# Optimization experiments

Hardware: AMD Instinct MI355X
Metric: run time of the kernel (lower is better)

The kernel has to match this reference:

```python
import jax, jax.numpy as jnp
import numpy as np

B, HIS, SIG, DIM, K = 16, 50, 512, 256, 8


def setup_inputs() -> dict:
    key = jax.random.key(0)
    ks = jax.random.split(key, 10)
    f = jax.random.normal
    return {
        "news_selection_embedding": f(ks[0], (B, HIS, SIG, DIM), jnp.float32),
        "news_embedding": f(ks[1], (B, HIS, SIG, DIM), jnp.float32),
        "user_repr": f(ks[2], (B, 1, DIM), jnp.float32),
        "news_repr": f(ks[3], (B, HIS, DIM), jnp.float32),
        "his_attn_mask": jax.random.randint(ks[4], (B, HIS, SIG), 0, 2, jnp.int32),
        "his_refined_mask": jax.random.randint(ks[5], (B, HIS, SIG), 0, 2, jnp.int32),
        "W_align": f(ks[6], (DIM, 2 * DIM), jnp.float32) * 0.05,
        "b_align": jnp.zeros((DIM,), jnp.float32),
        "sep_embedding": f(ks[7], (1, 1, 1, DIM), jnp.float32),
        "order_embedding": f(ks[8], (HIS, 1, DIM), jnp.float32),
    }


def _l2norm(x, axis):
    # F.normalize: x / clamp_min(||x||, 1e-12)
    n = jnp.linalg.norm(x, axis=axis, keepdims=True)
    return x / jnp.maximum(n, 1e-12)


def reference(news_selection_embedding, news_embedding, user_repr, news_repr,
              his_attn_mask, his_refined_mask, W_align, b_align,
              sep_embedding, order_embedding):
    Bs, H, S, D = news_embedding.shape
    # drop the leading [CLS]-style token
    sel = news_selection_embedding[:, :, 1:]          # [B,H,S-1,D]
    emb = news_embedding[:, :, 1:]                    # [B,H,S-1,D]

    # diversify: selection query from concat(user, news) through Linear(2D->D)
    nu = jnp.concatenate([jnp.broadcast_to(user_repr, news_repr.shape), news_repr], axis=-1)
    query = nu @ W_align.T + b_align                  # [B,H,D]

    # cosine similarity scores
    scores = jnp.einsum('bhsd,bhd->bhs', _l2norm(sel, -1), _l2norm(query, -1))

    # keep first k tokens always selectable; mask padded positions
    keep_k = jnp.zeros((1, S), scores.dtype).at[:, :K + 1].set(1.0)
    pad_pos = (his_refined_mask.astype(scores.dtype) + keep_k)[:, :, 1:] == 0
    scores = jnp.where(pad_pos, -jnp.inf, scores)

    score_k, kid = jax.lax.top_k(scores, K)           # [B,H,K]

    # dual gather: embeddings and attention mask
    ps_terms = jnp.take_along_axis(emb, kid[..., None], axis=2)             # [B,H,K,D]
    ps_term_mask = jnp.take_along_axis(
        his_attn_mask[:, :, 1:].astype(scores.dtype), kid, axis=-1)         # [B,H,K]

    # softmax weighting (threshold == -inf path)
    ps_terms = ps_terms * jax.nn.softmax(score_k, axis=-1)[..., None]

    # order embedding + [SEP] per article, flatten, drop trailing sep
    ps_terms = ps_terms + order_embedding             # [H,1,D] broadcast
    sep = jnp.broadcast_to(sep_embedding, (Bs, H, 1, D))
    ps_terms = jnp.concatenate([ps_terms, sep], axis=2).reshape(Bs, -1, D)[:, :-1]
    ones = jnp.ones((Bs, H, 1), ps_term_mask.dtype)
    ps_term_mask = jnp.concatenate([ps_term_mask, ones], axis=-1).reshape(Bs, -1)[:, :-1]
    return ps_terms, ps_term_mask, kid
```

## Files before the change

kernel.cpp:

```cpp
#include <hip/hip_runtime.h>
#include <math.h>

constexpr int NB  = 16;
constexpr int NH  = 50;
constexpr int NS  = 512;
constexpr int ND  = 256;
constexpr int NK  = 8;
constexpr int SM1 = NS - 1;
constexpr int ROWS = NH * (NK + 1) - 1;
constexpr int HB  = 5;
constexpr int CHUNKS = 4;
constexpr int RPC = 128;

template<int CTRL>
__device__ __forceinline__ float dpp_add(float v) {
    const int p = __builtin_amdgcn_update_dpp(0, __float_as_int(v), CTRL, 0xF, 0xF, true);
    return v + __int_as_float(p);
}

__device__ __forceinline__ float dpp_reduce16(float v) {
    v = dpp_add<0xB1>(v);
    v = dpp_add<0x4E>(v);
    v = dpp_add<0x141>(v);
    v = dpp_add<0x140>(v);
    return v;
}

__device__ __forceinline__ float4 ntload4(const float* p) {
    typedef float f4v __attribute__((ext_vector_type(4)));
    const f4v v = __builtin_nontemporal_load((const f4v*)p);
    float4 r; r.x = v.x; r.y = v.y; r.z = v.z; r.w = v.w;
    return r;
}

__global__ __launch_bounds__(256) void query_kernel(
    const float* __restrict__ user,
    const float* __restrict__ news_repr,
    const float* __restrict__ W,
    const float* __restrict__ bal,
    float* __restrict__ qn)
{
    __shared__ float us[ND];
    __shared__ float nr[HB][ND];
    __shared__ float qv_s[HB][ND];
    __shared__ float red[4];

    const int blk = blockIdx.x;
    const int b   = blk / (NH / HB);
    const int h0  = (blk % (NH / HB)) * HB;
    const int tid = threadIdx.x;
    const int ql  = tid & 15;
    const int q   = tid >> 4;

    us[tid] = user[b * ND + tid];
    #pragma unroll
    for (int i = 0; i < HB; ++i)
        nr[i][tid] = news_repr[((size_t)(b * NH + h0 + i)) * ND + tid];
    __syncthreads();

    for (int p = 0; p < 16; ++p) {
        const int d = p * 16 + q;
        const float* wrow = W + (size_t)d * (2 * ND);
        float pu = 0.f;
        float pa[HB];
        #pragma unroll
        for (int j = 0; j < HB; ++j) pa[j] = 0.f;

        #pragma unroll
        for (int i = 0; i < 4; ++i) {
            const int e = ql * 4 + 64 * i;
            const float4 wv = *(const float4*)(wrow + e);
            const float4 xv = *(const float4*)(us + e);
            pu += wv.x * xv.x + wv.y * xv.y + wv.z * xv.z + wv.w * xv.w;
        }
        #pragma unroll
        for (int i = 0; i < 4; ++i) {
            const int e = ql * 4 + 64 * i;
            const float4 wv = *(const float4*)(wrow + ND + e);
            #pragma unroll
            for (int j = 0; j < HB; ++j) {
                const float4 xv = *(const float4*)(&nr[j][e]);
                pa[j] += wv.x * xv.x + wv.y * xv.y + wv.z * xv.z + wv.w * xv.w;
            }
        }

        pu = dpp_reduce16(pu);
        #pragma unroll
        for (int j = 0; j < HB; ++j) pa[j] = dpp_reduce16(pa[j]);

        if (ql == 0) {
            const float base = bal[d] + pu;
            #pragma unroll
            for (int j = 0; j < HB; ++j) qv_s[j][d] = base + pa[j];
        }
    }
    __syncthreads();

    const int lane = tid & 63, wv_ = tid >> 6;
    for (int j = 0; j < HB; ++j) {
        const float v = qv_s[j][tid];
        float sq = v * v;
        #pragma unroll
        for (int m = 1; m < 64; m <<= 1) sq += __shfl_xor(sq, m, 64);
        if (lane == 0) red[wv_] = sq;
        __syncthreads();
        const float tot = red[0] + red[1] + red[2] + red[3];
        __syncthreads();
        qn[((size_t)(b * NH + h0 + j)) * ND + tid] = v / fmaxf(sqrtf(tot), 1e-12f);
    }
}

__global__ __launch_bounds__(256, 8) void score_kernel(
    const float* __restrict__ sel,
    const float* __restrict__ qn,
    float* __restrict__ scw)
{
    __shared__ float qs[ND];

    const int blk   = blockIdx.x;
    const int bh    = blk >> 2;
    const int chunk = blk & (CHUNKS - 1);
    const int j0    = chunk * RPC;
    const int tid   = threadIdx.x;
    const int ql    = tid & 15;
    const int q     = tid >> 4;

    qs[tid] = qn[(size_t)bh * ND + tid];
    __syncthreads();

    const float* base_bh = sel + (size_t)bh * NS * ND;

    #pragma unroll 2
    for (int it = 0; it < 8; ++it) {
        const int j = j0 + q + it * 16;
        const bool valid = (j < SM1);
        const int s = valid ? (j + 1) : SM1;
        const float* row = base_bh + (size_t)s * ND;
        float dot = 0.f, nrm = 0.f;
        #pragma unroll
        for (int i = 0; i < 4; ++i) {
            const float4 v  = ntload4(row + i * 64 + ql * 4);
            const float4 qv = *(const float4*)(qs + i * 64 + ql * 4);
            dot += v.x * qv.x + v.y * qv.y + v.z * qv.z + v.w * qv.w;
            nrm += v.x * v.x + v.y * v.y + v.z * v.z + v.w * v.w;
        }
        dot = dpp_reduce16(dot);
        nrm = dpp_reduce16(nrm);

        if (valid && ql == 0)
            scw[(size_t)bh * NS + j] = dot / fmaxf(sqrtf(nrm), 1e-12f);
    }
}

__global__ __launch_bounds__(64) void topk_out_kernel(
    const float* __restrict__ emb,
    const int*   __restrict__ attn,
    const int*   __restrict__ refined,
    const float* __restrict__ scw,
    const float* __restrict__ sep,
    const float* __restrict__ orde,
    float* __restrict__ out_terms,
    float* __restrict__ out_mask,
    float* __restrict__ out_kid)
{
    const int bh   = blockIdx.x;
    const int b    = bh / NH, h = bh % NH;
    const int lane = threadIdx.x;

    float v[8];
    {
        const float4 a = *(const float4*)(scw + (size_t)bh * NS + lane * 8);
        const float4 c = *(const float4*)(scw + (size_t)bh * NS + lane * 8 + 4);
        v[0] = a.x; v[1] = a.y; v[2] = a.z; v[3] = a.w;
        v[4] = c.x; v[5] = c.y; v[6] = c.z; v[7] = c.w;
    }
    #pragma unroll
    for (int t = 0; t < 8; ++t) {
        const int j = lane * 8 + t;
        if (j >= SM1)
            v[t] = -INFINITY;
        else if (j >= NK && refined[(size_t)bh * NS + j + 1] == 0)
            v[t] = -INFINITY;
    }

    float topv[NK];
    int   topi[NK];
    int   myi = 0;
    #pragma unroll
    for (int k = 0; k < NK; ++k) {
        float bv = -INFINITY; int bi = 0x7fffffff;
        #pragma unroll
        for (int t = 0; t < 8; ++t)
            if (v[t] > bv) { bv = v[t]; bi = lane * 8 + t; }
        #pragma unroll
        for (int m = 1; m < 64; m <<= 1) {
            const float ov = __shfl_xor(bv, m, 64);
            const int   oi = __shfl_xor(bi, m, 64);
            if (ov > bv || (ov == bv && oi < bi)) { bv = ov; bi = oi; }
        }
        topv[k] = bv; topi[k] = bi;
        if (lane == k) myi = bi;
        #pragma unroll
        for (int t = 0; t < 8; ++t)
            if (lane * 8 + t == bi) v[t] = -INFINITY;
    }

    float wk[NK], ssum = 0.f;
    #pragma unroll
    for (int k = 0; k < NK; ++k) { wk[k] = expf(topv[k] - topv[0]); ssum += wk[k]; }
    const float inv = 1.f / ssum;

    const int d4 = lane * 4;
    const float4 ord4 = *(const float4*)(orde + (size_t)h * ND + d4);
    float* obase = out_terms + ((size_t)b * ROWS + h * (NK + 1)) * ND;
    #pragma unroll
    for (int k = 0; k < NK; ++k) {
        const int s = topi[k] + 1;
        const float4 e = *(const float4*)(emb + ((size_t)bh * NS + s) * ND + d4);
        const float w = wk[k] * inv;
        float4 o;
        o.x = e.x * w + ord4.x;
        o.y = e.y * w + ord4.y;
        o.z = e.z * w + ord4.z;
        o.w = e.w * w + ord4.w;
        *(float4*)(obase + k * ND + d4) = o;
    }
    const bool has_sep = h < NH - 1;
    if (has_sep)
        *(float4*)(obase + NK * ND + d4) = *(const float4*)(sep + d4);

    if (lane < NK) {
        out_mask[(size_t)b * ROWS + h * (NK + 1) + lane] =
            (float)attn[(size_t)bh * NS + myi + 1];
        out_kid[(size_t)bh * NK + lane] = (float)myi;
    }
    if (lane == NK && has_sep)
        out_mask[(size_t)b * ROWS + h * (NK + 1) + NK] = 1.0f;
}

extern "C" void kernel_launch(void* const* d_in, const int* in_sizes, int n_in,
                              void* d_out, int out_size, void* d_ws, size_t ws_size,
                              hipStream_t stream) {
    const float* sel   = (const float*)d_in[0];
    const float* emb   = (const float*)d_in[1];
    const float* user  = (const float*)d_in[2];
    const float* nrp   = (const float*)d_in[3];
    const int*   attn  = (const int*)d_in[4];
    const int*   refin = (const int*)d_in[5];
    const float* W     = (const float*)d_in[6];
    const float* bal   = (const float*)d_in[7];
    const float* sep   = (const float*)d_in[8];
    const float* orde  = (const float*)d_in[9];

    float* qn  = (float*)d_ws;
    float* scw = qn + (size_t)NB * NH * ND;

    float* out_terms = (float*)d_out;
    float* out_mask  = out_terms + (size_t)NB * ROWS * ND;
    float* out_kid   = out_mask + (size_t)NB * ROWS;

    query_kernel<<<NB * (NH / HB), 256, 0, stream>>>(user, nrp, W, bal, qn);
    score_kernel<<<NB * NH * CHUNKS, 256, 0, stream>>>(sel, qn, scw);
    topk_out_kernel<<<NB * NH, 64, 0, stream>>>(emb, attn, refin, scw, sep, orde,
                                                out_terms, out_mask, out_kid);
}
```

Baseline: 94.21 us.

## Fuse query projection, scoring, top-k and gather into one per-head kernel

Replaces the three launches (query matvec, chunked cosine scoring, top-k/gather) with a single kernel that runs one 256-thread block per (batch, history) pair. Scores stay in shared memory instead of a workspace round-trip, and the query norm is folded into each score as one multiply. The aim is to drop the launch gaps and the intermediate global traffic. In exchange, each block now reads the whole W matrix on its own, where before one read served five heads, and the score phase runs with a quarter as many blocks, with fewer loads in flight to stream the large selection tensor.

```diff
diff --git a/kernel.cpp b/kernel.cpp
--- a/kernel.cpp
+++ b/kernel.cpp
@@ -8,9 +8,6 @@
 constexpr int NK  = 8;
 constexpr int SM1 = NS - 1;
 constexpr int ROWS = NH * (NK + 1) - 1;
-constexpr int HB  = 5;
-constexpr int CHUNKS = 4;
-constexpr int RPC = 128;
 
 template<int CTRL>
 __device__ __forceinline__ float dpp_add(float v) {
@@ -33,209 +30,167 @@
     return r;
 }
 
-__global__ __launch_bounds__(256) void query_kernel(
+__global__ __launch_bounds__(256, 8) void fused_kernel(
+    const float* __restrict__ sel,
+    const float* __restrict__ emb,
     const float* __restrict__ user,
-    const float* __restrict__ news_repr,
+    const float* __restrict__ nrp,
+    const int*   __restrict__ attn,
+    const int*   __restrict__ refined,
     const float* __restrict__ W,
     const float* __restrict__ bal,
-    float* __restrict__ qn)
-{
-    __shared__ float us[ND];
-    __shared__ float nr[HB][ND];
-    __shared__ float qv_s[HB][ND];
-    __shared__ float red[4];
-
-    const int blk = blockIdx.x;
-    const int b   = blk / (NH / HB);
-    const int h0  = (blk % (NH / HB)) * HB;
-    const int tid = threadIdx.x;
-    const int ql  = tid & 15;
-    const int q   = tid >> 4;
-
-    us[tid] = user[b * ND + tid];
-    #pragma unroll
-    for (int i = 0; i < HB; ++i)
-        nr[i][tid] = news_repr[((size_t)(b * NH + h0 + i)) * ND + tid];
-    __syncthreads();
-
-    for (int p = 0; p < 16; ++p) {
-        const int d = p * 16 + q;
-        const float* wrow = W + (size_t)d * (2 * ND);
-        float pu = 0.f;
-        float pa[HB];
-        #pragma unroll
-        for (int j = 0; j < HB; ++j) pa[j] = 0.f;
-
-        #pragma unroll
-        for (int i = 0; i < 4; ++i) {
-            const int e = ql * 4 + 64 * i;
-            const float4 wv = *(const float4*)(wrow + e);
-            const float4 xv = *(const float4*)(us + e);
-            pu += wv.x * xv.x + wv.y * xv.y + wv.z * xv.z + wv.w * xv.w;
-        }
-        #pragma unroll
-        for (int i = 0; i < 4; ++i) {
-            const int e = ql * 4 + 64 * i;
-            const float4 wv = *(const float4*)(wrow + ND + e);
-            #pragma unroll
-            for (int j = 0; j < HB; ++j) {
-                const float4 xv = *(const float4*)(&nr[j][e]);
-                pa[j] += wv.x * xv.x + wv.y * xv.y + wv.z * xv.z + wv.w * xv.w;
-            }
-        }
-
-        pu = dpp_reduce16(pu);
-        #pragma unroll
-        for (int j = 0; j < HB; ++j) pa[j] = dpp_reduce16(pa[j]);
-
-        if (ql == 0) {
-            const float base = bal[d] + pu;
-            #pragma unroll
-            for (int j = 0; j < HB; ++j) qv_s[j][d] = base + pa[j];
-        }
-    }
-    __syncthreads();
-
-    const int lane = tid & 63, wv_ = tid >> 6;
-    for (int j = 0; j < HB; ++j) {
-        const float v = qv_s[j][tid];
-        float sq = v * v;
-        #pragma unroll
-        for (int m = 1; m < 64; m <<= 1) sq += __shfl_xor(sq, m, 64);
-        if (lane == 0) red[wv_] = sq;
-        __syncthreads();
-        const float tot = red[0] + red[1] + red[2] + red[3];
-        __syncthreads();
-        qn[((size_t)(b * NH + h0 + j)) * ND + tid] = v / fmaxf(sqrtf(tot), 1e-12f);
-    }
-}
-
-__global__ __launch_bounds__(256, 8) void score_kernel(
-    const float* __restrict__ sel,
-    const float* __restrict__ qn,
-    float* __restrict__ scw)
-{
-    __shared__ float qs[ND];
-
-    const int blk   = blockIdx.x;
-    const int bh    = blk >> 2;
-    const int chunk = blk & (CHUNKS - 1);
-    const int j0    = chunk * RPC;
-    const int tid   = threadIdx.x;
-    const int ql    = tid & 15;
-    const int q     = tid >> 4;
-
-    qs[tid] = qn[(size_t)bh * ND + tid];
-    __syncthreads();
-
-    const float* base_bh = sel + (size_t)bh * NS * ND;
-
-    #pragma unroll 2
-    for (int it = 0; it < 8; ++it) {
-        const int j = j0 + q + it * 16;
-        const bool valid = (j < SM1);
-        const int s = valid ? (j + 1) : SM1;
-        const float* row = base_bh + (size_t)s * ND;
-        float dot = 0.f, nrm = 0.f;
-        #pragma unroll
-        for (int i = 0; i < 4; ++i) {
-            const float4 v  = ntload4(row + i * 64 + ql * 4);
-            const float4 qv = *(const float4*)(qs + i * 64 + ql * 4);
-            dot += v.x * qv.x + v.y * qv.y + v.z * qv.z + v.w * qv.w;
-            nrm += v.x * v.x + v.y * v.y + v.z * v.z + v.w * v.w;
-        }
-        dot = dpp_reduce16(dot);
-        nrm = dpp_reduce16(nrm);
-
-        if (valid && ql == 0)
-            scw[(size_t)bh * NS + j] = dot / fmaxf(sqrtf(nrm), 1e-12f);
-    }
-}
-
-__global__ __launch_bounds__(64) void topk_out_kernel(
-    const float* __restrict__ emb,
-    const int*   __restrict__ attn,
-    const int*   __restrict__ refined,
-    const float* __restrict__ scw,
     const float* __restrict__ sep,
     const float* __restrict__ orde,
     float* __restrict__ out_terms,
     float* __restrict__ out_mask,
     float* __restrict__ out_kid)
 {
+    __shared__ float xs[2 * ND];
+    __shared__ float qs[ND];
+    __shared__ float sc_s[NS];
+    __shared__ float red[4];
+    __shared__ float qinv_sh;
+    __shared__ int   kid_sh[NK];
+    __shared__ float wgt_sh[NK];
+
     const int bh   = blockIdx.x;
     const int b    = bh / NH, h = bh % NH;
-    const int lane = threadIdx.x;
-
-    float v[8];
+    const int tid  = threadIdx.x;
+    const int ql   = tid & 15;
+    const int q    = tid >> 4;
+    const int lane = tid & 63, wv = tid >> 6;
+
+    xs[tid]      = user[(size_t)b * ND + tid];
+    xs[ND + tid] = nrp[(size_t)bh * ND + tid];
+    __syncthreads();
+
+    for (int p = 0; p < 16; ++p) {
+        const int d = p * 16 + q;
+        const float* wrow = W + (size_t)d * (2 * ND);
+        float acc = 0.f;
+        #pragma unroll
+        for (int i = 0; i < 8; ++i) {
+            const int e = ql * 4 + 64 * i;
+            const float4 wvv = *(const float4*)(wrow + e);
+            const float4 xv  = *(const float4*)(xs + e);
+            acc += wvv.x * xv.x + wvv.y * xv.y + wvv.z * xv.z + wvv.w * xv.w;
+        }
+        acc = dpp_reduce16(acc);
+        if (ql == 0) qs[d] = bal[d] + acc;
+    }
+    __syncthreads();
+
     {
-        const float4 a = *(const float4*)(scw + (size_t)bh * NS + lane * 8);
-        const float4 c = *(const float4*)(scw + (size_t)bh * NS + lane * 8 + 4);
-        v[0] = a.x; v[1] = a.y; v[2] = a.z; v[3] = a.w;
-        v[4] = c.x; v[5] = c.y; v[6] = c.z; v[7] = c.w;
-    }
-    #pragma unroll
-    for (int t = 0; t < 8; ++t) {
-        const int j = lane * 8 + t;
-        if (j >= SM1)
-            v[t] = -INFINITY;
-        else if (j >= NK && refined[(size_t)bh * NS + j + 1] == 0)
-            v[t] = -INFINITY;
-    }
-
-    float topv[NK];
-    int   topi[NK];
-    int   myi = 0;
-    #pragma unroll
-    for (int k = 0; k < NK; ++k) {
-        float bv = -INFINITY; int bi = 0x7fffffff;
-        #pragma unroll
-        for (int t = 0; t < 8; ++t)
-            if (v[t] > bv) { bv = v[t]; bi = lane * 8 + t; }
-        #pragma unroll
-        for (int m = 1; m < 64; m <<= 1) {
-            const float ov = __shfl_xor(bv, m, 64);
-            const int   oi = __shfl_xor(bi, m, 64);
-            if (ov > bv || (ov == bv && oi < bi)) { bv = ov; bi = oi; }
-        }
-        topv[k] = bv; topi[k] = bi;
-        if (lane == k) myi = bi;
-        #pragma unroll
-        for (int t = 0; t < 8; ++t)
-            if (lane * 8 + t == bi) v[t] = -INFINITY;
-    }
-
-    float wk[NK], ssum = 0.f;
-    #pragma unroll
-    for (int k = 0; k < NK; ++k) { wk[k] = expf(topv[k] - topv[0]); ssum += wk[k]; }
-    const float inv = 1.f / ssum;
+        const float v = qs[tid];
+        float sq = v * v;
+        #pragma unroll
+        for (int m = 1; m < 64; m <<= 1) sq += __shfl_xor(sq, m, 64);
+        if (lane == 0) red[wv] = sq;
+        __syncthreads();
+        if (tid == 0)
+            qinv_sh = 1.f / fmaxf(sqrtf(red[0] + red[1] + red[2] + red[3]), 1e-12f);
+        __syncthreads();
+    }
+    const float qinv = qinv_sh;
+
+    const float* base_bh = sel + (size_t)bh * NS * ND;
+    #pragma unroll 2
+    for (int it = 0; it < 32; ++it) {
+        const int j = q + it * 16;
+        const bool valid = (j < SM1);
+        const int s = valid ? (j + 1) : SM1;
+        const float* row = base_bh + (size_t)s * ND;
+        float dot = 0.f, nrm = 0.f;
+        #pragma unroll
+        for (int i = 0; i < 4; ++i) {
+            const float4 v  = ntload4(row + i * 64 + ql * 4);
+            const float4 qv = *(const float4*)(qs + i * 64 + ql * 4);
+            dot += v.x * qv.x + v.y * qv.y + v.z * qv.z + v.w * qv.w;
+            nrm += v.x * v.x + v.y * v.y + v.z * v.z + v.w * v.w;
+        }
+        dot = dpp_reduce16(dot);
+        nrm = dpp_reduce16(nrm);
+        if (valid && ql == 0)
+            sc_s[j] = dot * qinv / fmaxf(sqrtf(nrm), 1e-12f);
+    }
+    __syncthreads();
+
+    if (wv == 0) {
+        float v[8];
+        #pragma unroll
+        for (int t = 0; t < 8; ++t) {
+            const int j = lane * 8 + t;
+            float x = sc_s[j];
+            if (j >= SM1)
+                x = -INFINITY;
+            else if (j >= NK && refined[(size_t)bh * NS + j + 1] == 0)
+                x = -INFINITY;
+            v[t] = x;
+        }
+
+        float topv[NK];
+        int   topi[NK];
+        int   myi = 0;
+        #pragma unroll
+        for (int k = 0; k < NK; ++k) {
+            float bv = -INFINITY; int bi = 0x7fffffff;
+            #pragma unroll
+            for (int t = 0; t < 8; ++t)
+                if (v[t] > bv) { bv = v[t]; bi = lane * 8 + t; }
+            #pragma unroll
+            for (int m = 1; m < 64; m <<= 1) {
+                const float ov = __shfl_xor(bv, m, 64);
+                const int   oi = __shfl_xor(bi, m, 64);
+                if (ov > bv || (ov == bv && oi < bi)) { bv = ov; bi = oi; }
+            }
+            topv[k] = bv; topi[k] = bi;
+            if (lane == k) myi = bi;
+            #pragma unroll
+            for (int t = 0; t < 8; ++t)
+                if (lane * 8 + t == bi) v[t] = -INFINITY;
+        }
+
+        float wk[NK], ssum = 0.f;
+        #pragma unroll
+        for (int k = 0; k < NK; ++k) { wk[k] = expf(topv[k] - topv[0]); ssum += wk[k]; }
+        const float inv = 1.f / ssum;
+
+        if (lane == 0) {
+            #pragma unroll
+            for (int k = 0; k < NK; ++k) {
+                kid_sh[k] = topi[k];
+                wgt_sh[k] = wk[k] * inv;
+            }
+        }
+
+        if (lane < NK) {
+            out_mask[(size_t)b * ROWS + h * (NK + 1) + lane] =
+                (float)attn[(size_t)bh * NS + myi + 1];
+            out_kid[(size_t)bh * NK + lane] = (float)myi;
+        }
+        if (lane == NK && h < NH - 1)
+            out_mask[(size_t)b * ROWS + h * (NK + 1) + NK] = 1.0f;
+    }
+    __syncthreads();
 
     const int d4 = lane * 4;
     const float4 ord4 = *(const float4*)(orde + (size_t)h * ND + d4);
     float* obase = out_terms + ((size_t)b * ROWS + h * (NK + 1)) * ND;
-    #pragma unroll
-    for (int k = 0; k < NK; ++k) {
-        const int s = topi[k] + 1;
-        const float4 e = *(const float4*)(emb + ((size_t)bh * NS + s) * ND + d4);
-        const float w = wk[k] * inv;
-        float4 o;
-        o.x = e.x * w + ord4.x;
-        o.y = e.y * w + ord4.y;
-        o.z = e.z * w + ord4.z;
-        o.w = e.w * w + ord4.w;
-        *(float4*)(obase + k * ND + d4) = o;
-    }
-    const bool has_sep = h < NH - 1;
-    if (has_sep)
-        *(float4*)(obase + NK * ND + d4) = *(const float4*)(sep + d4);
-
-    if (lane < NK) {
-        out_mask[(size_t)b * ROWS + h * (NK + 1) + lane] =
-            (float)attn[(size_t)bh * NS + myi + 1];
-        out_kid[(size_t)bh * NK + lane] = (float)myi;
-    }
-    if (lane == NK && has_sep)
-        out_mask[(size_t)b * ROWS + h * (NK + 1) + NK] = 1.0f;
+    for (int r = wv; r < NK + 1; r += 4) {
+        if (r < NK) {
+            const int s2 = kid_sh[r] + 1;
+            const float4 e = *(const float4*)(emb + ((size_t)bh * NS + s2) * ND + d4);
+            const float w = wgt_sh[r];
+            float4 o;
+            o.x = e.x * w + ord4.x;
+            o.y = e.y * w + ord4.y;
+            o.z = e.z * w + ord4.z;
+            o.w = e.w * w + ord4.w;
+            *(float4*)(obase + r * ND + d4) = o;
+        } else if (h < NH - 1) {
+            *(float4*)(obase + NK * ND + d4) = *(const float4*)(sep + d4);
+        }
+    }
 }
 
 extern "C" void kernel_launch(void* const* d_in, const int* in_sizes, int n_in,
@@ -252,15 +207,11 @@
     const float* sep   = (const float*)d_in[8];
     const float* orde  = (const float*)d_in[9];
 
-    float* qn  = (float*)d_ws;
-    float* scw = qn + (size_t)NB * NH * ND;
-
     float* out_terms = (float*)d_out;
     float* out_mask  = out_terms + (size_t)NB * ROWS * ND;
     float* out_kid   = out_mask + (size_t)NB * ROWS;
 
-    query_kernel<<<NB * (NH / HB), 256, 0, stream>>>(user, nrp, W, bal, qn);
-    score_kernel<<<NB * NH * CHUNKS, 256, 0, stream>>>(sel, qn, scw);
-    topk_out_kernel<<<NB * NH, 64, 0, stream>>>(emb, attn, refin, scw, sep, orde,
-                                                out_terms, out_mask, out_kid);
-}
+    fused_kernel<<<NB * NH, 256, 0, stream>>>(sel, emb, user, nrp, attn, refin,
+                                              W, bal, sep, orde,
+                                              out_terms, out_mask, out_kid);
+}
```

New measurement: 98.88 us. 5.0% more time.

## Fuse score and top-k/gather kernels into one block per (b,h)

Applied to the files above, without the earlier changes.

Merges the cosine-score kernel and the top-k/gather/output kernel into a single kernel with one 256-thread block per (batch, history) pair. Scores stay in shared memory instead of round-tripping through a global workspace, and one kernel launch is dropped. In exchange, the grid shrinks from 3200 to 800 blocks, each streaming a full 512-row selection slice. The top-k stage runs on a single wave while the other three sit idle, which may reduce memory-level parallelism on the dominant 134MB read.

```diff
diff --git a/kernel.cpp b/kernel.cpp
--- a/kernel.cpp
+++ b/kernel.cpp
@@ -9,8 +9,6 @@
 constexpr int SM1 = NS - 1;
 constexpr int ROWS = NH * (NK + 1) - 1;
 constexpr int HB  = 5;
-constexpr int CHUNKS = 4;
-constexpr int RPC = 128;
 
 template<int CTRL>
 __device__ __forceinline__ float dpp_add(float v) {
@@ -110,132 +108,131 @@
     }
 }
 
-__global__ __launch_bounds__(256, 8) void score_kernel(
+__global__ __launch_bounds__(256, 8) void score_topk_kernel(
     const float* __restrict__ sel,
-    const float* __restrict__ qn,
-    float* __restrict__ scw)
-{
-    __shared__ float qs[ND];
-
-    const int blk   = blockIdx.x;
-    const int bh    = blk >> 2;
-    const int chunk = blk & (CHUNKS - 1);
-    const int j0    = chunk * RPC;
-    const int tid   = threadIdx.x;
-    const int ql    = tid & 15;
-    const int q     = tid >> 4;
-
-    qs[tid] = qn[(size_t)bh * ND + tid];
-    __syncthreads();
-
-    const float* base_bh = sel + (size_t)bh * NS * ND;
-
-    #pragma unroll 2
-    for (int it = 0; it < 8; ++it) {
-        const int j = j0 + q + it * 16;
-        const bool valid = (j < SM1);
-        const int s = valid ? (j + 1) : SM1;
-        const float* row = base_bh + (size_t)s * ND;
-        float dot = 0.f, nrm = 0.f;
-        #pragma unroll
-        for (int i = 0; i < 4; ++i) {
-            const float4 v  = ntload4(row + i * 64 + ql * 4);
-            const float4 qv = *(const float4*)(qs + i * 64 + ql * 4);
-            dot += v.x * qv.x + v.y * qv.y + v.z * qv.z + v.w * qv.w;
-            nrm += v.x * v.x + v.y * v.y + v.z * v.z + v.w * v.w;
-        }
-        dot = dpp_reduce16(dot);
-        nrm = dpp_reduce16(nrm);
-
-        if (valid && ql == 0)
-            scw[(size_t)bh * NS + j] = dot / fmaxf(sqrtf(nrm), 1e-12f);
-    }
-}
-
-__global__ __launch_bounds__(64) void topk_out_kernel(
     const float* __restrict__ emb,
     const int*   __restrict__ attn,
     const int*   __restrict__ refined,
-    const float* __restrict__ scw,
+    const float* __restrict__ qn,
     const float* __restrict__ sep,
     const float* __restrict__ orde,
     float* __restrict__ out_terms,
     float* __restrict__ out_mask,
     float* __restrict__ out_kid)
 {
+    __shared__ float qs[ND];
+    __shared__ float sc_s[NS];
+    __shared__ int   kid_sh[NK];
+    __shared__ float wgt_sh[NK];
+
     const int bh   = blockIdx.x;
     const int b    = bh / NH, h = bh % NH;
-    const int lane = threadIdx.x;
-
-    float v[8];
-    {
-        const float4 a = *(const float4*)(scw + (size_t)bh * NS + lane * 8);
-        const float4 c = *(const float4*)(scw + (size_t)bh * NS + lane * 8 + 4);
-        v[0] = a.x; v[1] = a.y; v[2] = a.z; v[3] = a.w;
-        v[4] = c.x; v[5] = c.y; v[6] = c.z; v[7] = c.w;
-    }
-    #pragma unroll
-    for (int t = 0; t < 8; ++t) {
-        const int j = lane * 8 + t;
-        if (j >= SM1)
-            v[t] = -INFINITY;
-        else if (j >= NK && refined[(size_t)bh * NS + j + 1] == 0)
-            v[t] = -INFINITY;
-    }
-
-    float topv[NK];
-    int   topi[NK];
-    int   myi = 0;
-    #pragma unroll
-    for (int k = 0; k < NK; ++k) {
-        float bv = -INFINITY; int bi = 0x7fffffff;
-        #pragma unroll
-        for (int t = 0; t < 8; ++t)
-            if (v[t] > bv) { bv = v[t]; bi = lane * 8 + t; }
-        #pragma unroll
-        for (int m = 1; m < 64; m <<= 1) {
-            const float ov = __shfl_xor(bv, m, 64);
-            const int   oi = __shfl_xor(bi, m, 64);
-            if (ov > bv || (ov == bv && oi < bi)) { bv = ov; bi = oi; }
-        }
-        topv[k] = bv; topi[k] = bi;
-        if (lane == k) myi = bi;
-        #pragma unroll
-        for (int t = 0; t < 8; ++t)
-            if (lane * 8 + t == bi) v[t] = -INFINITY;
-    }
-
-    float wk[NK], ssum = 0.f;
-    #pragma unroll
-    for (int k = 0; k < NK; ++k) { wk[k] = expf(topv[k] - topv[0]); ssum += wk[k]; }
-    const float inv = 1.f / ssum;
+    const int tid  = threadIdx.x;
+    const int ql   = tid & 15;
+    const int q    = tid >> 4;
+    const int lane = tid & 63, wv = tid >> 6;
+
+    qs[tid] = qn[(size_t)bh * ND + tid];
+    __syncthreads();
+
+    const float* base_bh = sel + (size_t)bh * NS * ND;
+    #pragma unroll 2
+    for (int it = 0; it < 32; ++it) {
+        const int j = q + it * 16;
+        const bool valid = (j < SM1);
+        const int s = valid ? (j + 1) : SM1;
+        const float* row = base_bh + (size_t)s * ND;
+        float dot = 0.f, nrm = 0.f;
+        #pragma unroll
+        for (int i = 0; i < 4; ++i) {
+            const float4 v  = ntload4(row + i * 64 + ql * 4);
+            const float4 qv = *(const float4*)(qs + i * 64 + ql * 4);
+            dot += v.x * qv.x + v.y * qv.y + v.z * qv.z + v.w * qv.w;
+            nrm += v.x * v.x + v.y * v.y + v.z * v.z + v.w * v.w;
+        }
+        dot = dpp_reduce16(dot);
+        nrm = dpp_reduce16(nrm);
+        if (valid && ql == 0)
+            sc_s[j] = dot / fmaxf(sqrtf(nrm), 1e-12f);
+    }
+    __syncthreads();
+
+    if (wv == 0) {
+        float v[8];
+        #pragma unroll
+        for (int t = 0; t < 8; ++t) {
+            const int j = lane * 8 + t;
+            float x = sc_s[j];
+            if (j >= SM1)
+                x = -INFINITY;
+            else if (j >= NK && refined[(size_t)bh * NS + j + 1] == 0)
+                x = -INFINITY;
+            v[t] = x;
+        }
+
+        float topv[NK];
+        int   topi[NK];
+        int   myi = 0;
+        #pragma unroll
+        for (int k = 0; k < NK; ++k) {
+            float bv = -INFINITY; int bi = 0x7fffffff;
+            #pragma unroll
+            for (int t = 0; t < 8; ++t)
+                if (v[t] > bv) { bv = v[t]; bi = lane * 8 + t; }
+            #pragma unroll
+            for (int m = 1; m < 64; m <<= 1) {
+                const float ov = __shfl_xor(bv, m, 64);
+                const int   oi = __shfl_xor(bi, m, 64);
+                if (ov > bv || (ov == bv && oi < bi)) { bv = ov; bi = oi; }
+            }
+            topv[k] = bv; topi[k] = bi;
+            if (lane == k) myi = bi;
+            #pragma unroll
+            for (int t = 0; t < 8; ++t)
+                if (lane * 8 + t == bi) v[t] = -INFINITY;
+        }
+
+        float wk[NK], ssum = 0.f;
+        #pragma unroll
+        for (int k = 0; k < NK; ++k) { wk[k] = expf(topv[k] - topv[0]); ssum += wk[k]; }
+        const float inv = 1.f / ssum;
+
+        if (lane == 0) {
+            #pragma unroll
+            for (int k = 0; k < NK; ++k) {
+                kid_sh[k] = topi[k];
+                wgt_sh[k] = wk[k] * inv;
+            }
+        }
+
+        if (lane < NK) {
+            out_mask[(size_t)b * ROWS + h * (NK + 1) + lane] =
+                (float)attn[(size_t)bh * NS + myi + 1];
+            out_kid[(size_t)bh * NK + lane] = (float)myi;
+        }
+        if (lane == NK && h < NH - 1)
+            out_mask[(size_t)b * ROWS + h * (NK + 1) + NK] = 1.0f;
+    }
+    __syncthreads();
 
     const int d4 = lane * 4;
     const float4 ord4 = *(const float4*)(orde + (size_t)h * ND + d4);
     float* obase = out_terms + ((size_t)b * ROWS + h * (NK + 1)) * ND;
-    #pragma unroll
-    for (int k = 0; k < NK; ++k) {
-        const int s = topi[k] + 1;
-        const float4 e = *(const float4*)(emb + ((size_t)bh * NS + s) * ND + d4);
-        const float w = wk[k] * inv;
-        float4 o;
-        o.x = e.x * w + ord4.x;
-        o.y = e.y * w + ord4.y;
-        o.z = e.z * w + ord4.z;
-        o.w = e.w * w + ord4.w;
-        *(float4*)(obase + k * ND + d4) = o;
-    }
-    const bool has_sep = h < NH - 1;
-    if (has_sep)
-        *(float4*)(obase + NK * ND + d4) = *(const float4*)(sep + d4);
-
-    if (lane < NK) {
-        out_mask[(size_t)b * ROWS + h * (NK + 1) + lane] =
-            (float)attn[(size_t)bh * NS + myi + 1];
-        out_kid[(size_t)bh * NK + lane] = (float)myi;
-    }
-    if (lane == NK && has_sep)
-        out_mask[(size_t)b * ROWS + h * (NK + 1) + NK] = 1.0f;
+    for (int r = wv; r < NK + 1; r += 4) {
+        if (r < NK) {
+            const int s2 = kid_sh[r] + 1;
+            const float4 e = *(const float4*)(emb + ((size_t)bh * NS + s2) * ND + d4);
+            const float w = wgt_sh[r];
+            float4 o;
+            o.x = e.x * w + ord4.x;
+            o.y = e.y * w + ord4.y;
+            o.z = e.z * w + ord4.z;
+            o.w = e.w * w + ord4.w;
+            *(float4*)(obase + r * ND + d4) = o;
+        } else if (h < NH - 1) {
+            *(float4*)(obase + NK * ND + d4) = *(const float4*)(sep + d4);
+        }
+    }
 }
 
 extern "C" void kernel_launch(void* const* d_in, const int* in_sizes, int n_in,
@@ -252,15 +249,14 @@
     const float* sep   = (const float*)d_in[8];
     const float* orde  = (const float*)d_in[9];
 
-    float* qn  = (float*)d_ws;
-    float* scw = qn + (size_t)NB * NH * ND;
+    float* qn = (float*)d_ws;
 
     float* out_terms = (float*)d_out;
     float* out_mask  = out_terms + (size_t)NB * ROWS * ND;
     float* out_kid   = out_mask + (size_t)NB * ROWS;
 
     query_kernel<<<NB * (NH / HB), 256, 0, stream>>>(user, nrp, W, bal, qn);
-    score_kernel<<<NB * NH * CHUNKS, 256, 0, stream>>>(sel, qn, scw);
-    topk_out_kernel<<<NB * NH, 64, 0, stream>>>(emb, attn, refin, scw, sep, orde,
-                                                out_terms, out_mask, out_kid);
-}
+    score_topk_kernel<<<NB * NH, 256, 0, stream>>>(sel, emb, attn, refin, qn,
+                                                   sep, orde,
+                                                   out_terms, out_mask, out_kid);
+}
```

Result: slower. 96.80 us (+2.7%).
